# Optimization experiments

Measured on AMD Instinct MI355X. Metric: run time of the kernel, lower is better.

The kernel has to match this reference:

```python
import jax, jax.numpy as jnp
import numpy as np

T, B, D, H = 512, 64, 1024, 8
DH = D // H
LN_EPS = 1e-5


def setup_inputs() -> dict:
    ks = jax.random.split(jax.random.key(0), 12)
    s = 1.0 / np.sqrt(D)
    return {
        "x_real": jax.random.normal(ks[0], (T, B, D), jnp.float32),
        "x_imag": jax.random.normal(ks[1], (T, B, D), jnp.float32),
        "value_state": jnp.zeros((B, H, DH), jnp.float32),
        "t": jnp.arange(T, dtype=jnp.int64) if jax.config.jax_enable_x64 else jnp.arange(T, dtype=jnp.int32),
        # ComplexLinear input_proj (bias=True): weight layout [out, in] like torch
        "Wr_in": jax.random.normal(ks[2], (D, D), jnp.float32) * s,
        "Wi_in": jax.random.normal(ks[3], (D, D), jnp.float32) * s,
        "br_in": jax.random.normal(ks[4], (D,), jnp.float32) * 0.01,
        "bi_in": jax.random.normal(ks[5], (D,), jnp.float32) * 0.01,
        # LayerNorm affine
        "ln_gamma": jnp.ones((D,), jnp.float32),
        "ln_beta": jnp.zeros((D,), jnp.float32),
        # QKV linear (bias=False), torch layout [3D, D]
        "W_qkv": jax.random.normal(ks[6], (3 * D, D), jnp.float32) * s,
        # per-head EMA gate logits: log(alpha/(1-alpha)) with alpha=0.9
        "log_alpha": jnp.full((H,), float(np.log(0.9 / 0.1)), jnp.float32),
        # ComplexLinear output_proj (bias=False)
        "Wr_out": jax.random.normal(ks[7], (D, D), jnp.float32) * s,
        "Wi_out": jax.random.normal(ks[8], (D, D), jnp.float32) * s,
    }


def reference(x_real, x_imag, value_state, t, Wr_in, Wi_in, br_in, bi_in,
              ln_gamma, ln_beta, W_qkv, log_alpha, Wr_out, Wi_out):
    scale = jnp.asarray(np.sqrt(DH), x_real.dtype)
    alpha = jax.nn.sigmoid(log_alpha)[None, :, None]  # [1,H,1]

    def step(state, xs):
        xr, xi = xs  # [B,D] each
        # ComplexLinear input projection
        pr = xr @ Wr_in.T - xi @ Wi_in.T + br_in
        pi = xr @ Wi_in.T + xi @ Wr_in.T + bi_in
        xc = pr + pi
        # LayerNorm over last dim
        mu = xc.mean(-1, keepdims=True)
        var = ((xc - mu) ** 2).mean(-1, keepdims=True)
        xc = (xc - mu) * jax.lax.rsqrt(var + LN_EPS) * ln_gamma + ln_beta
        # QKV
        qkv = (xc @ W_qkv.T).reshape(-1, 3, H, DH)
        q, k, v = qkv[:, 0], qkv[:, 1], qkv[:, 2]  # [B,H,DH]
        # per-head sigmoid-gated EMA state update
        new_state = alpha * v + (1.0 - alpha) * state
        gate = jax.nn.sigmoid(jnp.sum(q * k, axis=-1, keepdims=True) / scale)  # [B,H,1]
        retrieved = (gate * new_state).reshape(-1, D)
        # ComplexLinear output projection with zero imaginary input
        return new_state, (retrieved @ Wr_out.T, retrieved @ Wi_out.T)

    final_state, (out_real, out_imag) = jax.lax.scan(step, value_state, (x_real, x_imag))
    return out_real, out_imag, final_state
```

## Files before the change

kernel.cpp:

```cpp
#include <hip/hip_runtime.h>
#include <stdint.h>

#define T_DIM 512
#define B_DIM 64
#define D_DIM 1024
#define H_DIM 8
#define DH_DIM 128
#define MROWS (T_DIM * B_DIM)

typedef unsigned short u16;
typedef __attribute__((ext_vector_type(8))) __bf16 bf16x8;
typedef __attribute__((ext_vector_type(4))) float f32x4;
typedef __attribute__((ext_vector_type(16))) float f32x16;

__device__ __forceinline__ u16 f2bf(float f) {
  union { float f; uint32_t u; } v; v.f = f;
  uint32_t u = v.u;
  u += 0x7fffu + ((u >> 16) & 1u);
  return (u16)(u >> 16);
}
__device__ __forceinline__ float bf2f(u16 h) {
  union { uint32_t u; float f; } v; v.u = ((uint32_t)h) << 16;
  return v.f;
}

__device__ __forceinline__ void gload16(const void* g, void* l) {
  __builtin_amdgcn_global_load_lds(
      (const __attribute__((address_space(1))) uint32_t*)g,
      (__attribute__((address_space(3))) uint32_t*)l, 16, 0, 0);
}

#define SB()  __builtin_amdgcn_sched_barrier(0)
#define BAR() __builtin_amdgcn_s_barrier()
#define VM4() asm volatile("s_waitcnt vmcnt(4)" ::: "memory")
#define VM6() asm volatile("s_waitcnt vmcnt(6)" ::: "memory")
#define VM12() asm volatile("s_waitcnt vmcnt(12)" ::: "memory")
#define LGK0() asm volatile("s_waitcnt lgkmcnt(0)" ::: "memory")
#define PRIO1() __builtin_amdgcn_s_setprio(1)
#define PRIO0() __builtin_amdgcn_s_setprio(0)


__device__ __forceinline__ void cast8(const float* __restrict__ in, u16* __restrict__ out, size_t i) {
  const float4 a = ((const float4*)in)[i * 2];
  const float4 b = ((const float4*)in)[i * 2 + 1];
  union { u16 h[8]; uint4 u; } o;
  o.h[0] = f2bf(a.x); o.h[1] = f2bf(a.y); o.h[2] = f2bf(a.z); o.h[3] = f2bf(a.w);
  o.h[4] = f2bf(b.x); o.h[5] = f2bf(b.y); o.h[6] = f2bf(b.z); o.h[7] = f2bf(b.w);
  ((uint4*)out)[i] = o.u;
}

__global__ void prep_cast_kernel(const float* __restrict__ Wr, const float* __restrict__ Wi,
                                 const float* __restrict__ br, const float* __restrict__ bi,
                                 const float* __restrict__ Wqkv,
                                 const float* __restrict__ Wro, const float* __restrict__ Wio,
                                 u16* __restrict__ Wc, float* __restrict__ bc,
                                 u16* __restrict__ Wqkvb, u16* __restrict__ Wob) {
  const int blk = blockIdx.x;
  if (blk < 8192) {
    const int idx = blk * 256 + threadIdx.x;
    const int n = idx >> 11;
    const int k = idx & 2047;
    const int kk = k & 1023;
    const float a = Wr[n * 1024 + kk], b = Wi[n * 1024 + kk];
    Wc[idx] = f2bf(k < 1024 ? a + b : a - b);
  } else if (blk < 9728) {
    cast8(Wqkv, Wqkvb, (size_t)(blk - 8192) * 256 + threadIdx.x);
  } else if (blk < 10240) {
    cast8(Wro, Wob, (size_t)(blk - 9728) * 256 + threadIdx.x);
  } else if (blk < 10752) {
    cast8(Wio, Wob + (size_t)1024 * 1024, (size_t)(blk - 10240) * 256 + threadIdx.x);
  } else {
    const int i = (blk - 10752) * 256 + threadIdx.x;
    if (i < D_DIM) bc[i] = br[i] + bi[i];
  }
}


__device__ __forceinline__ void readF(bf16x8 (&d)[2][2], const u16* s, int rowoff, int la32, int puA) {
#pragma unroll
  for (int mf = 0; mf < 2; ++mf)
#pragma unroll
    for (int kk = 0; kk < 2; ++kk)
      d[mf][kk] = *(const bf16x8*)(s + (rowoff + mf * 32 + la32) * 32 + (puA ^ (kk << 4)));
}

__device__ __forceinline__ void mfma8(f32x16 (&acc)[4][2], const bf16x8 (&a)[2][2],
                                      const bf16x8 (&b)[2][2], int QM) {
#pragma unroll
  for (int kk = 0; kk < 2; ++kk)
#pragma unroll
    for (int mf = 0; mf < 2; ++mf)
#pragma unroll
      for (int nf = 0; nf < 2; ++nf)
        acc[QM * 2 + mf][nf] =
            __builtin_amdgcn_mfma_f32_32x32x16_bf16(a[mf][kk], b[nf][kk], acc[QM * 2 + mf][nf], 0, 0, 0);
}

__global__ __launch_bounds__(512, 2) void gemm_f32a_kernel(
    const float* __restrict__ A0f, const float* __restrict__ A1f, int kSplit, int lda,
    const u16* __restrict__ Bw, int ldb,
    const float* __restrict__ bias,
    u16* __restrict__ C0, int ldc, int K, int nColBlk)
{
  extern __shared__ u16 lds[];
  const int tid  = threadIdx.x;
  const int lane = tid & 63;
  const int w    = tid >> 6;
  const int wr   = w >> 2;
  const int wc   = w & 3;

  const int bid   = blockIdx.x;
  const int xcd   = bid & 7;
  const int local = bid >> 3;
  const int rowL  = local / nColBlk;
  const int colB  = local - rowL * nColBlk;
  const size_t rowBase = (size_t)(xcd * 16 + rowL) * 256;
  const size_t colBase = (size_t)colB * 256;

  f32x16 acc[4][2];
#pragma unroll
  for (int i = 0; i < 4; ++i)
#pragma unroll
    for (int j = 0; j < 2; ++j)
#pragma unroll
      for (int e = 0; e < 16; ++e) acc[i][j][e] = 0.f;

  const int NT = K >> 6;
  const int la32 = lane & 31;
  const int g2   = lane >> 5;
  const int f    = (la32 & 3) ^ ((la32 >> 2) & 3);
  const int puA  = ((g2 ^ f) << 3);

  float4 ar[8];

  auto aload = [&](int t) {
    if (t >= NT) t = 0;
    const int kb = t * 64;
    const float* Af; int kc;
    if (kb < kSplit) { Af = A0f; kc = kb; } else { Af = A1f; kc = kb - kSplit; }
#pragma unroll
    for (int ks = 0; ks < 2; ++ks)
#pragma unroll
      for (int i2 = 0; i2 < 2; ++i2) {
        const int l = i2 * 512 + tid, r = l >> 2, p = l & 3;
        const int lu = p ^ (r & 3) ^ ((r >> 2) & 3);
        const float* g = Af + (rowBase + r) * (size_t)lda + kc + ks * 32 + lu * 8;
        ar[ks * 4 + i2 * 2 + 0] = *(const float4*)g;
        ar[ks * 4 + i2 * 2 + 1] = *(const float4*)(g + 4);
      }
  };
  auto cwrite = [&](int buf) {
#pragma unroll
    for (int ks = 0; ks < 2; ++ks)
#pragma unroll
      for (int i2 = 0; i2 < 2; ++i2) {
        const int l = i2 * 512 + tid;
        const float4 x0 = ar[ks * 4 + i2 * 2 + 0];
        const float4 x1 = ar[ks * 4 + i2 * 2 + 1];
        union { u16 h[8]; uint4 u; } o;
        o.h[0] = f2bf(x0.x); o.h[1] = f2bf(x0.y); o.h[2] = f2bf(x0.z); o.h[3] = f2bf(x0.w);
        o.h[4] = f2bf(x1.x); o.h[5] = f2bf(x1.y); o.h[6] = f2bf(x1.z); o.h[7] = f2bf(x1.w);
        *(uint4*)(lds + buf * 32768 + ks * 8192 + (size_t)l * 8) = o.u;
      }
  };
  auto bgload = [&](int buf, int t) {
    if (t >= NT) t = 0;
    const int kb = t * 64;
#pragma unroll
    for (int ks = 0; ks < 2; ++ks)
#pragma unroll
      for (int i2 = 0; i2 < 2; ++i2) {
        const int l = i2 * 512 + tid, r = l >> 2, p = l & 3;
        const int lu = p ^ (r & 3) ^ ((r >> 2) & 3);
        gload16(Bw + (colBase + r) * (size_t)ldb + kb + ks * 32 + lu * 8,
                lds + buf * 32768 + 16384 + ks * 8192 + (size_t)l * 8);
      }
  };

  const int rA0 = wr * 128;
  const int rA1 = wr * 128 + 64;
  const int rB  = wc * 64;

  aload(0);
  bgload(0, 0);
  cwrite(0);
  aload(1);
  bgload(1, 1);
  SB(); VM12(); LGK0(); BAR(); SB();

  bf16x8 a0[2][2], a1[2][2], bb[2][2];
  for (int t = 0; t < NT; ++t) {
    const int cur = t & 1, o = cur ^ 1;
    const u16* sA = lds + cur * 32768;
    const u16* sBt = lds + cur * 32768 + 16384;
    readF(a0, sA, rA0, la32, puA);
    readF(a1, sA, rA1, la32, puA);
    readF(bb, sBt, rB, la32, puA);
    PRIO1(); mfma8(acc, a0, bb, 0); mfma8(acc, a1, bb, 1); PRIO0();
    readF(a0, sA + 8192, rA0, la32, puA);
    readF(a1, sA + 8192, rA1, la32, puA);
    readF(bb, sBt + 8192, rB, la32, puA);
    PRIO1(); mfma8(acc, a0, bb, 0); mfma8(acc, a1, bb, 1); PRIO0();
    SB(); BAR(); SB();
    cwrite(o);
    aload(t + 2);
    bgload(cur, t + 2);
    SB(); VM12(); LGK0(); BAR(); SB();
  }

#pragma unroll
  for (int mi = 0; mi < 4; ++mi)
#pragma unroll
    for (int ni = 0; ni < 2; ++ni) {
      const int cn = wc * 64 + ni * 32 + la32;
      const float badd = bias[colBase + cn];
      const size_t col = colBase + cn;
#pragma unroll
      for (int r = 0; r < 16; ++r) {
        const size_t row = rowBase + wr * 128 + mi * 32 + (r & 3) + 8 * (r >> 2) + 4 * g2;
        C0[row * (size_t)ldc + col] = f2bf(acc[mi][ni][r] + badd);
      }
    }
}


template <int EPI>
__global__ __launch_bounds__(512, 2) void gemm256_kernel(
    const u16* __restrict__ A0, const u16* __restrict__ A1, int kSplit, int lda,
    const u16* __restrict__ Bw, int ldb,
    const float* __restrict__ bias,
    void* __restrict__ C0, void* __restrict__ C1, void* __restrict__ C2,
    int ldc, int K, int nColBlk)
{
  extern __shared__ u16 lds[];
  const int tid  = threadIdx.x;
  const int lane = tid & 63;
  const int w    = tid >> 6;
  const int wr   = w >> 2;
  const int wc   = w & 3;

  const int bid   = blockIdx.x;
  const int xcd   = bid & 7;
  const int local = bid >> 3;
  const int rowL  = local / nColBlk;
  const int colB  = local - rowL * nColBlk;
  const size_t rowBase = (size_t)(xcd * 16 + rowL) * 256;
  const size_t colBase = (size_t)colB * 256;

  f32x16 acc[4][2];
#pragma unroll
  for (int i = 0; i < 4; ++i)
#pragma unroll
    for (int j = 0; j < 2; ++j)
#pragma unroll
      for (int e = 0; e < 16; ++e) acc[i][j][e] = 0.f;

  const int NT = K >> 6;
  const int la32 = lane & 31;
  const int g2   = lane >> 5;
  const int f    = (la32 & 3) ^ ((la32 >> 2) & 3);
  const int puA  = ((g2 ^ f) << 3);

  auto stageA = [&](int buf, int ks, int t) {
    if (t >= NT) t = 0;
    const int kb = t * 64;
    const u16* Ab; int kc;
    if (kb < kSplit) { Ab = A0; kc = kb; } else { Ab = A1; kc = kb - kSplit; }
    u16* dst = lds + buf * 32768 + ks * 8192;
#pragma unroll
    for (int i2 = 0; i2 < 2; ++i2) {
      const int l = i2 * 512 + tid, r = l >> 2, p = l & 3;
      const int lu = p ^ (r & 3) ^ ((r >> 2) & 3);
      gload16(Ab + (rowBase + r) * (size_t)lda + kc + ks * 32 + lu * 8, dst + l * 8);
    }
  };
  auto stageB = [&](int buf, int ks, int t) {
    if (t >= NT) t = 0;
    const int kb = t * 64;
    u16* dst = lds + buf * 32768 + 16384 + ks * 8192;
#pragma unroll
    for (int i2 = 0; i2 < 2; ++i2) {
      const int l = i2 * 512 + tid, r = l >> 2, p = l & 3;
      const int lu = p ^ (r & 3) ^ ((r >> 2) & 3);
      gload16(Bw + (colBase + r) * (size_t)ldb + kb + ks * 32 + lu * 8, dst + l * 8);
    }
  };

  const u16* sA_b0k0 = lds;
  const u16* sA_b0k1 = lds + 8192;
  const u16* sB_b0k0 = lds + 16384;
  const u16* sB_b0k1 = lds + 16384 + 8192;
  const u16* sA_b1k0 = lds + 32768;
  const u16* sA_b1k1 = lds + 32768 + 8192;
  const u16* sB_b1k0 = lds + 32768 + 16384;
  const u16* sB_b1k1 = lds + 32768 + 16384 + 8192;
  const int rA0 = wr * 128;
  const int rA1 = wr * 128 + 64;
  const int rB  = wc * 64;

  stageA(0, 0, 0); stageB(0, 0, 0); stageA(0, 1, 0); stageB(0, 1, 0);
  stageA(1, 0, 1); stageB(1, 0, 1);
  VM4();
  SB(); BAR(); SB();

  bf16x8 a0[2][2], a1[2][2], bbE[2][2], bbO[2][2];
  const int NIT = NT >> 1;
  for (int i = 0; i < NIT; ++i) {
    const int u = 2 * i, v = 2 * i + 1;
    readF(a0,  sA_b0k0, rA0, la32, puA);
    readF(bbE, sB_b0k0, rB,  la32, puA);
    readF(a1,  sA_b0k0, rA1, la32, puA);
    stageA(1, 1, v);
    SB(); BAR(); SB();
    PRIO1(); mfma8(acc, a0, bbE, 0); PRIO0(); SB();
    BAR(); SB();
    readF(a0,  sA_b0k1, rA0, la32, puA);
    readF(bbO, sB_b0k1, rB,  la32, puA);
    stageB(1, 1, v);
    SB(); BAR(); SB();
    PRIO1(); mfma8(acc, a1, bbE, 1); PRIO0(); SB();
    BAR(); SB();
    readF(a1,  sA_b0k1, rA1, la32, puA);
    stageA(0, 0, u + 2);
    SB(); BAR(); SB();
    PRIO1(); mfma8(acc, a0, bbO, 0); PRIO0(); SB();
    VM6();
    BAR(); SB();
    readF(a0,  sA_b1k0, rA0, la32, puA);
    readF(bbE, sB_b1k0, rB,  la32, puA);
    stageB(0, 0, u + 2);
    SB(); BAR(); SB();
    PRIO1(); mfma8(acc, a1, bbO, 1); PRIO0(); SB();
    VM4();
    BAR(); SB();
    readF(a1,  sA_b1k0, rA1, la32, puA);
    stageA(0, 1, u + 2);
    SB(); BAR(); SB();
    PRIO1(); mfma8(acc, a0, bbE, 0); PRIO0(); SB();
    BAR(); SB();
    readF(a0,  sA_b1k1, rA0, la32, puA);
    readF(bbO, sB_b1k1, rB,  la32, puA);
    stageB(0, 1, u + 2);
    SB(); BAR(); SB();
    PRIO1(); mfma8(acc, a1, bbE, 1); PRIO0(); SB();
    BAR(); SB();
    readF(a1,  sA_b1k1, rA1, la32, puA);
    stageA(1, 0, v + 2);
    SB(); BAR(); SB();
    PRIO1(); mfma8(acc, a0, bbO, 0); PRIO0(); SB();
    BAR(); SB();
    stageB(1, 0, v + 2);
    SB(); BAR(); SB();
    PRIO1(); mfma8(acc, a1, bbO, 1); PRIO0(); SB();
    VM4();
    BAR(); SB();
  }

  const int seg = (int)(colBase >> 10);
  const size_t colSeg = colBase & 1023;
  void* Cout;
  if (EPI == 3)      Cout = (seg == 0) ? C0 : (seg == 1) ? C1 : C2;
  else if (EPI == 2) Cout = (seg == 0) ? C0 : C1;
  else               Cout = C0;

#pragma unroll
  for (int mi = 0; mi < 4; ++mi)
#pragma unroll
    for (int ni = 0; ni < 2; ++ni) {
      const int cn = wc * 64 + ni * 32 + la32;
      const float badd = (EPI == 1) ? bias[colBase + cn] : 0.0f;
      const size_t col = colSeg + cn;
#pragma unroll
      for (int r = 0; r < 16; ++r) {
        const size_t row = rowBase + wr * 128 + mi * 32 + (r & 3) + 8 * (r >> 2) + 4 * g2;
        const float v = acc[mi][ni][r] + badd;
        if (EPI == 2) ((float*)Cout)[row * (size_t)ldc + col] = v;
        else          ((u16*)Cout)[row * (size_t)ldc + col] = f2bf(v);
      }
    }
}


__global__ __launch_bounds__(256) void ln_kernel(u16* __restrict__ xc,
    const float* __restrict__ gamma, const float* __restrict__ beta)
{
  const size_t row = blockIdx.x;
  u16* p = xc + row * D_DIM;
  const int tid = threadIdx.x;
  const int c = tid * 4;
  const uint2 raw = *(const uint2*)(p + c);
  const float v0 = bf2f((u16)(raw.x & 0xffff)), v1 = bf2f((u16)(raw.x >> 16));
  const float v2 = bf2f((u16)(raw.y & 0xffff)), v3 = bf2f((u16)(raw.y >> 16));
  float s = v0 + v1 + v2 + v3;
  float q = v0 * v0 + v1 * v1 + v2 * v2 + v3 * v3;
#pragma unroll
  for (int o = 32; o > 0; o >>= 1) { s += __shfl_xor(s, o); q += __shfl_xor(q, o); }
  __shared__ float red[8];
  if ((tid & 63) == 0) { red[(tid >> 6) * 2] = s; red[(tid >> 6) * 2 + 1] = q; }
  __syncthreads();
  s = red[0] + red[2] + red[4] + red[6];
  q = red[1] + red[3] + red[5] + red[7];
  const float mu = s * (1.0f / D_DIM);
  const float var = q * (1.0f / D_DIM) - mu * mu;
  const float rstd = 1.0f / sqrtf(var + 1e-5f);
  const float y0 = (v0 - mu) * rstd * gamma[c] + beta[c];
  const float y1 = (v1 - mu) * rstd * gamma[c + 1] + beta[c + 1];
  const float y2 = (v2 - mu) * rstd * gamma[c + 2] + beta[c + 2];
  const float y3 = (v3 - mu) * rstd * gamma[c + 3] + beta[c + 3];
  const uint32_t o0 = (uint32_t)f2bf(y0) | ((uint32_t)f2bf(y1) << 16);
  const uint32_t o1 = (uint32_t)f2bf(y2) | ((uint32_t)f2bf(y3) << 16);
  *(uint2*)(p + c) = make_uint2(o0, o1);
}


__global__ __launch_bounds__(256) void gate_kernel(
    const u16* __restrict__ Q, const u16* __restrict__ Kb, float* __restrict__ gate)
{
  const int gw = blockIdx.x * 4 + (threadIdx.x >> 6);
  const int lane = threadIdx.x & 63;
  const size_t row = (size_t)(gw >> 3);
  const int h = gw & 7;
  const size_t off = row * D_DIM + h * DH_DIM + lane * 2;
  const uint32_t qr = *(const uint32_t*)(Q + off);
  const uint32_t kr = *(const uint32_t*)(Kb + off);
  float d = bf2f((u16)(qr & 0xffff)) * bf2f((u16)(kr & 0xffff))
          + bf2f((u16)(qr >> 16))    * bf2f((u16)(kr >> 16));
#pragma unroll
  for (int o = 32; o > 0; o >>= 1) d += __shfl_xor(d, o);
  if (lane == 0) {
    const float x = d * 0.08838834764831845f;
    gate[gw] = 1.0f / (1.0f + expf(-x));
  }
}


__global__ __launch_bounds__(256) void scan1_kernel(
    const u16* __restrict__ vb, const float* __restrict__ log_alpha,
    float* __restrict__ carry)
{
  const int j  = blockIdx.x >> 7;
  const int th = (blockIdx.x & 127) * 256 + threadIdx.x;
  const int gid = th * 2;
  const int b = gid >> 10;
  const int c = gid & 1023;
  const int h = c >> 7;
  const float alpha = 1.0f / (1.0f + expf(-log_alpha[h]));
  const float oma = 1.0f - alpha;
  const u16* vp = vb + ((size_t)(4096 * j + b)) * 1024 + c;
  float s0 = 0.f, s1 = 0.f;
#pragma unroll 8
  for (int i = 0; i < 64; ++i) {
    const uint32_t uv = *(const uint32_t*)(vp + (size_t)i * 65536);
    s0 = alpha * bf2f((u16)(uv & 0xffff)) + oma * s0;
    s1 = alpha * bf2f((u16)(uv >> 16))    + oma * s1;
  }
  *(float2*)(carry + (size_t)j * 65536 + gid) = make_float2(s0, s1);
}

__global__ __launch_bounds__(256) void scan2_kernel(
    const u16* __restrict__ vb, const float* __restrict__ gate,
    const float* __restrict__ vstate, const float* __restrict__ log_alpha,
    const float* __restrict__ carry,
    u16* __restrict__ ret, float* __restrict__ fstate)
{
  const int j  = blockIdx.x >> 7;
  const int th = (blockIdx.x & 127) * 256 + threadIdx.x;
  const int gid = th * 2;
  const int b = gid >> 10;
  const int c = gid & 1023;
  const int h = c >> 7;
  const float alpha = 1.0f / (1.0f + expf(-log_alpha[h]));
  const float oma = 1.0f - alpha;
  float o64 = oma;
#pragma unroll
  for (int q = 0; q < 6; ++q) o64 *= o64;
  float s0 = vstate[gid], s1 = vstate[gid + 1];
  for (int i = 0; i < j; ++i) {
    const float2 L = *(const float2*)(carry + (size_t)i * 65536 + gid);
    s0 = L.x + o64 * s0;
    s1 = L.y + o64 * s1;
  }
  const u16* vp = vb + ((size_t)(4096 * j + b)) * 1024 + c;
  u16* rp = ret + ((size_t)(4096 * j + b)) * 1024 + c;
  const float* gp = gate + (size_t)(4096 * j + b) * H_DIM + h;
#pragma unroll 4
  for (int i = 0; i < 64; ++i) {
    const uint32_t uv = *(const uint32_t*)(vp + (size_t)i * 65536);
    const float g = gp[(size_t)i * 512];
    s0 = alpha * bf2f((u16)(uv & 0xffff)) + oma * s0;
    s1 = alpha * bf2f((u16)(uv >> 16))    + oma * s1;
    const uint32_t o = (uint32_t)f2bf(g * s0) | ((uint32_t)f2bf(g * s1) << 16);
    *(uint32_t*)(rp + (size_t)i * 65536) = o;
  }
  if (j == 7) { fstate[gid] = s0; fstate[gid + 1] = s1; }
}


extern "C" void kernel_launch(void* const* d_in, const int* in_sizes, int n_in,
                              void* d_out, int out_size, void* d_ws, size_t ws_size,
                              hipStream_t stream) {
  const float* x_real      = (const float*)d_in[0];
  const float* x_imag      = (const float*)d_in[1];
  const float* value_state = (const float*)d_in[2];
  const float* Wr_in  = (const float*)d_in[4];
  const float* Wi_in  = (const float*)d_in[5];
  const float* br_in  = (const float*)d_in[6];
  const float* bi_in  = (const float*)d_in[7];
  const float* ln_g   = (const float*)d_in[8];
  const float* ln_b   = (const float*)d_in[9];
  const float* W_qkv  = (const float*)d_in[10];
  const float* log_alpha = (const float*)d_in[11];
  const float* Wr_out = (const float*)d_in[12];
  const float* Wi_out = (const float*)d_in[13];

  float* out_real = (float*)d_out;
  float* out_imag = out_real + (size_t)MROWS * D_DIM;
  float* fstate   = out_imag + (size_t)MROWS * D_DIM;

  u16* R0a = (u16*)d_out;
  u16* xc  = (u16*)((char*)d_out + (size_t)MROWS * D_DIM * 2);
  u16* Vb  = (u16*)out_imag;

  char* ws = (char*)d_ws;
  size_t off = 0;
  auto alloc = [&](size_t bytes) { void* p = ws + off; off += (bytes + 255) & ~(size_t)255; return p; };
  u16*   Wc    = (u16*)alloc((size_t)1024 * 2048 * 2);
  u16*   Wqkvb = (u16*)alloc((size_t)3072 * 1024 * 2);
  u16*   Wob   = (u16*)alloc((size_t)2048 * 1024 * 2);
  float* bc    = (float*)alloc((size_t)D_DIM * 4);
  u16*   R0b   = (u16*)alloc((size_t)MROWS * D_DIM * 2);
  float* gate  = (float*)alloc((size_t)MROWS * H_DIM * 4);
  float* carry = (float*)alloc((size_t)8 * B_DIM * D_DIM * 4);

  const int LDSB = 131072;
  hipFuncSetAttribute((const void*)gemm_f32a_kernel,  hipFuncAttributeMaxDynamicSharedMemorySize, LDSB);
  hipFuncSetAttribute((const void*)gemm256_kernel<2>, hipFuncAttributeMaxDynamicSharedMemorySize, LDSB);
  hipFuncSetAttribute((const void*)gemm256_kernel<3>, hipFuncAttributeMaxDynamicSharedMemorySize, LDSB);

  prep_cast_kernel<<<10756, 256, 0, stream>>>(Wr_in, Wi_in, br_in, bi_in, W_qkv, Wr_out, Wi_out,
                                              Wc, bc, Wqkvb, Wob);

  gemm_f32a_kernel<<<dim3(128 * 4), 512, LDSB, stream>>>(
      x_real, x_imag, 1024, 1024, Wc, 2048, bc, xc, 1024, 2048, 4);
  ln_kernel<<<MROWS, 256, 0, stream>>>(xc, ln_g, ln_b);
  gemm256_kernel<3><<<dim3(128 * 12), 512, LDSB, stream>>>(
      xc, xc, 1024, 1024, Wqkvb, 1024, nullptr, R0a, R0b, Vb, 1024, 1024, 12);
  gate_kernel<<<(MROWS * H_DIM) / 4, 256, 0, stream>>>(R0a, R0b, gate);
  scan1_kernel<<<1024, 256, 0, stream>>>(Vb, log_alpha, carry);
  scan2_kernel<<<1024, 256, 0, stream>>>(Vb, gate, value_state, log_alpha, carry, R0b, fstate);
  gemm256_kernel<2><<<dim3(128 * 8), 512, LDSB, stream>>>(
      R0b, R0b, 1024, 1024, Wob, 1024, nullptr, out_real, out_imag, nullptr, 1024, 1024, 8);
}
```

Measured before the change: 701.3 us.

## Interleave half-tile A/B staging with MFMA phases in input-projection GEMM main loop

Rewrites the GEMM main loop to process two K-tiles per iteration and split each tile into half-K stages. Global loads, bf16 conversion writes to LDS and async B loads are interleaved between individual MFMA groups, each phase separated by barriers with finer vmcnt waits. The aim is to hide global load latency and LDS write traffic behind matrix math instead of staging everything after the compute. It adds many more barriers per iteration. It also assumes NT is even and depends on tight wait-count bookkeeping, which could be fragile.

```diff
diff --git a/kernel.cpp b/kernel.cpp
--- a/kernel.cpp
+++ b/kernel.cpp
@@ -34,7 +34,7 @@
 #define BAR() __builtin_amdgcn_s_barrier()
 #define VM4() asm volatile("s_waitcnt vmcnt(4)" ::: "memory")
 #define VM6() asm volatile("s_waitcnt vmcnt(6)" ::: "memory")
-#define VM12() asm volatile("s_waitcnt vmcnt(12)" ::: "memory")
+#define VM10() asm volatile("s_waitcnt vmcnt(10)" ::: "memory")
 #define LGK0() asm volatile("s_waitcnt lgkmcnt(0)" ::: "memory")
 #define PRIO1() __builtin_amdgcn_s_setprio(1)
 #define PRIO0() __builtin_amdgcn_s_setprio(0)
@@ -131,81 +131,123 @@
   const int f    = (la32 & 3) ^ ((la32 >> 2) & 3);
   const int puA  = ((g2 ^ f) << 3);
 
-  float4 ar[8];
-
-  auto aload = [&](int t) {
+  float4 arE[4], arO[4];
+
+  auto aloadH = [&](int ks, int t, auto& ar) {
     if (t >= NT) t = 0;
     const int kb = t * 64;
     const float* Af; int kc;
     if (kb < kSplit) { Af = A0f; kc = kb; } else { Af = A1f; kc = kb - kSplit; }
 #pragma unroll
-    for (int ks = 0; ks < 2; ++ks)
-#pragma unroll
-      for (int i2 = 0; i2 < 2; ++i2) {
-        const int l = i2 * 512 + tid, r = l >> 2, p = l & 3;
-        const int lu = p ^ (r & 3) ^ ((r >> 2) & 3);
-        const float* g = Af + (rowBase + r) * (size_t)lda + kc + ks * 32 + lu * 8;
-        ar[ks * 4 + i2 * 2 + 0] = *(const float4*)g;
-        ar[ks * 4 + i2 * 2 + 1] = *(const float4*)(g + 4);
-      }
+    for (int i2 = 0; i2 < 2; ++i2) {
+      const int l = i2 * 512 + tid, r = l >> 2, p = l & 3;
+      const int lu = p ^ (r & 3) ^ ((r >> 2) & 3);
+      const float* g = Af + (rowBase + r) * (size_t)lda + kc + ks * 32 + lu * 8;
+      ar[i2 * 2 + 0] = *(const float4*)g;
+      ar[i2 * 2 + 1] = *(const float4*)(g + 4);
+    }
   };
-  auto cwrite = [&](int buf) {
-#pragma unroll
-    for (int ks = 0; ks < 2; ++ks)
-#pragma unroll
-      for (int i2 = 0; i2 < 2; ++i2) {
-        const int l = i2 * 512 + tid;
-        const float4 x0 = ar[ks * 4 + i2 * 2 + 0];
-        const float4 x1 = ar[ks * 4 + i2 * 2 + 1];
-        union { u16 h[8]; uint4 u; } o;
-        o.h[0] = f2bf(x0.x); o.h[1] = f2bf(x0.y); o.h[2] = f2bf(x0.z); o.h[3] = f2bf(x0.w);
-        o.h[4] = f2bf(x1.x); o.h[5] = f2bf(x1.y); o.h[6] = f2bf(x1.z); o.h[7] = f2bf(x1.w);
-        *(uint4*)(lds + buf * 32768 + ks * 8192 + (size_t)l * 8) = o.u;
-      }
+  auto cwriteH = [&](int buf, int ks, auto& ar) {
+#pragma unroll
+    for (int i2 = 0; i2 < 2; ++i2) {
+      const int l = i2 * 512 + tid;
+      const float4 x0 = ar[i2 * 2 + 0];
+      const float4 x1 = ar[i2 * 2 + 1];
+      union { u16 h[8]; uint4 u; } o;
+      o.h[0] = f2bf(x0.x); o.h[1] = f2bf(x0.y); o.h[2] = f2bf(x0.z); o.h[3] = f2bf(x0.w);
+      o.h[4] = f2bf(x1.x); o.h[5] = f2bf(x1.y); o.h[6] = f2bf(x1.z); o.h[7] = f2bf(x1.w);
+      *(uint4*)(lds + buf * 32768 + ks * 8192 + (size_t)l * 8) = o.u;
+    }
   };
-  auto bgload = [&](int buf, int t) {
+  auto stageB = [&](int buf, int ks, int t) {
     if (t >= NT) t = 0;
     const int kb = t * 64;
-#pragma unroll
-    for (int ks = 0; ks < 2; ++ks)
-#pragma unroll
-      for (int i2 = 0; i2 < 2; ++i2) {
-        const int l = i2 * 512 + tid, r = l >> 2, p = l & 3;
-        const int lu = p ^ (r & 3) ^ ((r >> 2) & 3);
-        gload16(Bw + (colBase + r) * (size_t)ldb + kb + ks * 32 + lu * 8,
-                lds + buf * 32768 + 16384 + ks * 8192 + (size_t)l * 8);
-      }
+    u16* dst = lds + buf * 32768 + 16384 + ks * 8192;
+#pragma unroll
+    for (int i2 = 0; i2 < 2; ++i2) {
+      const int l = i2 * 512 + tid, r = l >> 2, p = l & 3;
+      const int lu = p ^ (r & 3) ^ ((r >> 2) & 3);
+      gload16(Bw + (colBase + r) * (size_t)ldb + kb + ks * 32 + lu * 8, dst + l * 8);
+    }
   };
 
+  const u16* sA_b0k0 = lds;
+  const u16* sA_b0k1 = lds + 8192;
+  const u16* sB_b0k0 = lds + 16384;
+  const u16* sB_b0k1 = lds + 16384 + 8192;
+  const u16* sA_b1k0 = lds + 32768;
+  const u16* sA_b1k1 = lds + 32768 + 8192;
+  const u16* sB_b1k0 = lds + 32768 + 16384;
+  const u16* sB_b1k1 = lds + 32768 + 16384 + 8192;
   const int rA0 = wr * 128;
   const int rA1 = wr * 128 + 64;
   const int rB  = wc * 64;
 
-  aload(0);
-  bgload(0, 0);
-  cwrite(0);
-  aload(1);
-  bgload(1, 1);
-  SB(); VM12(); LGK0(); BAR(); SB();
-
-  bf16x8 a0[2][2], a1[2][2], bb[2][2];
-  for (int t = 0; t < NT; ++t) {
-    const int cur = t & 1, o = cur ^ 1;
-    const u16* sA = lds + cur * 32768;
-    const u16* sBt = lds + cur * 32768 + 16384;
-    readF(a0, sA, rA0, la32, puA);
-    readF(a1, sA, rA1, la32, puA);
-    readF(bb, sBt, rB, la32, puA);
-    PRIO1(); mfma8(acc, a0, bb, 0); mfma8(acc, a1, bb, 1); PRIO0();
-    readF(a0, sA + 8192, rA0, la32, puA);
-    readF(a1, sA + 8192, rA1, la32, puA);
-    readF(bb, sBt + 8192, rB, la32, puA);
-    PRIO1(); mfma8(acc, a0, bb, 0); mfma8(acc, a1, bb, 1); PRIO0();
-    SB(); BAR(); SB();
-    cwrite(o);
-    aload(t + 2);
-    bgload(cur, t + 2);
-    SB(); VM12(); LGK0(); BAR(); SB();
+  aloadH(0, 0, arE); cwriteH(0, 0, arE);
+  aloadH(1, 0, arE); cwriteH(0, 1, arE);
+  aloadH(0, 1, arE); cwriteH(1, 0, arE);
+  stageB(0, 0, 0); stageB(0, 1, 0);
+  aloadH(1, 1, arE);
+  stageB(1, 0, 1);
+  VM6();
+  LGK0();
+  SB(); BAR(); SB();
+
+  bf16x8 a0[2][2], a1[2][2], bbE[2][2], bbO[2][2];
+  const int NIT = NT >> 1;
+  for (int i = 0; i < NIT; ++i) {
+    const int u = 2 * i, v = 2 * i + 1;
+    readF(a0,  sA_b0k0, rA0, la32, puA);
+    readF(bbE, sB_b0k0, rB,  la32, puA);
+    readF(a1,  sA_b0k0, rA1, la32, puA);
+    cwriteH(1, 1, arE);
+    aloadH(0, u + 2, arO);
+    SB(); LGK0(); BAR(); SB();
+    PRIO1(); mfma8(acc, a0, bbE, 0); PRIO0(); SB();
+    BAR(); SB();
+    readF(a0,  sA_b0k1, rA0, la32, puA);
+    readF(bbO, sB_b0k1, rB,  la32, puA);
+    stageB(1, 1, v);
+    SB(); BAR(); SB();
+    PRIO1(); mfma8(acc, a1, bbE, 1); PRIO0(); SB();
+    BAR(); SB();
+    readF(a1,  sA_b0k1, rA1, la32, puA);
+    cwriteH(0, 0, arO);
+    aloadH(1, u + 2, arE);
+    SB(); LGK0(); BAR(); SB();
+    PRIO1(); mfma8(acc, a0, bbO, 0); PRIO0(); SB();
+    VM10();
+    BAR(); SB();
+    readF(a0,  sA_b1k0, rA0, la32, puA);
+    readF(bbE, sB_b1k0, rB,  la32, puA);
+    stageB(0, 0, u + 2);
+    SB(); BAR(); SB();
+    PRIO1(); mfma8(acc, a1, bbO, 1); PRIO0(); SB();
+    VM6();
+    BAR(); SB();
+    readF(a1,  sA_b1k0, rA1, la32, puA);
+    cwriteH(0, 1, arE);
+    aloadH(0, v + 2, arO);
+    SB(); LGK0(); BAR(); SB();
+    PRIO1(); mfma8(acc, a0, bbE, 0); PRIO0(); SB();
+    BAR(); SB();
+    readF(a0,  sA_b1k1, rA0, la32, puA);
+    readF(bbO, sB_b1k1, rB,  la32, puA);
+    stageB(0, 1, u + 2);
+    SB(); BAR(); SB();
+    PRIO1(); mfma8(acc, a1, bbE, 1); PRIO0(); SB();
+    BAR(); SB();
+    readF(a1,  sA_b1k1, rA1, la32, puA);
+    cwriteH(1, 0, arO);
+    aloadH(1, v + 2, arE);
+    SB(); LGK0(); BAR(); SB();
+    PRIO1(); mfma8(acc, a0, bbO, 0); PRIO0(); SB();
+    BAR(); SB();
+    stageB(1, 0, v + 2);
+    SB(); BAR(); SB();
+    PRIO1(); mfma8(acc, a1, bbO, 1); PRIO0(); SB();
+    VM6();
+    BAR(); SB();
   }
 
 #pragma unroll
```

Result: slower. 817.8 us (+16.6%).
